# Kernel tuning notes

Measured on AMD Instinct MI355X. Metric: run time of the kernel, lower is better.

Reference implementation:

```python
import jax, jax.numpy as jnp
import numpy as np

D_MODEL = 1024
N_HEADS = 16
HEAD_DIM = D_MODEL // N_HEADS


def setup_inputs() -> dict:
    key = jax.random.key(0)
    ks = jax.random.split(key, 5)
    x = jax.random.normal(ks[0], (4, 2048, D_MODEL), dtype=jnp.float32)
    # qkv Linear: weight [3*d_model, d_model], bias [3*d_model]
    w_qkv = jax.random.normal(ks[1], (3 * D_MODEL, D_MODEL), dtype=jnp.float32) / np.sqrt(D_MODEL)
    b_qkv = jnp.zeros((3 * D_MODEL,), dtype=jnp.float32)
    w_out = jax.random.normal(ks[2], (D_MODEL, D_MODEL), dtype=jnp.float32) / np.sqrt(D_MODEL)
    b_out = jnp.zeros((D_MODEL,), dtype=jnp.float32)
    return {"x": x, "w_qkv": w_qkv, "b_qkv": b_qkv, "w_out": w_out, "b_out": b_out}


def reference(x, w_qkv, b_qkv, w_out, b_out):
    B, T, C = x.shape
    H, Dh = N_HEADS, HEAD_DIM
    qkv = x @ w_qkv.T + b_qkv                      # [B,T,3C]
    qkv = qkv.reshape(B, T, 3, H, Dh)
    q = jnp.transpose(qkv[:, :, 0], (0, 2, 1, 3))  # [B,H,T,Dh]
    k = jnp.transpose(qkv[:, :, 1], (0, 2, 1, 3))
    v = jnpp_transpose = jnp.transpose(qkv[:, :, 2], (0, 2, 1, 3))
    scale = 1.0 / np.sqrt(Dh).astype(np.float32)
    att = jnp.einsum('bhqd,bhkd->bhqk', q, k) * scale
    causal = jnp.tril(jnp.ones((T, T), dtype=bool))
    att = jnp.where(causal[None, None], att, -jnp.inf)
    att = jax.nn.softmax(att, axis=-1)
    head_out = jnp.einsum('bhqk,bhkd->bhqd', att, v)  # [B,H,T,Dh]
    out = jnp.transpose(head_out, (0, 2, 1, 3)).reshape(B, T, C)
    return out @ w_out.T + b_out
```

## Files before the change

kernel.cpp:

```cpp
#include <hip/hip_runtime.h>
#include <hip/hip_bf16.h>


#define D_MODEL 1024
#define N_HEADS 16
#define HEAD_DIM 64
#define SEQ 2048
#define BATCH 4

typedef __attribute__((ext_vector_type(8))) short bf16x8;
typedef __attribute__((ext_vector_type(4))) float f32x4;
typedef unsigned int uint;

__device__ __forceinline__ short f2bf(float f) {
    union { float f; uint i; } c; c.f = f;
    uint x = c.i;
    x += 0x7fffu + ((x >> 16) & 1u);
    return (short)(x >> 16);
}
__device__ __forceinline__ uint pack2(float a, float b) {
    return (uint)(unsigned short)f2bf(a) | ((uint)(unsigned short)f2bf(b) << 16);
}

__device__ __forceinline__ void glds16(const void* g, void* l) {
    __builtin_amdgcn_global_load_lds(
        (const __attribute__((address_space(1))) uint*)g,
        (__attribute__((address_space(3))) uint*)l, 16, 0, 0);
}

__global__ __launch_bounds__(256) void cvt_bf16(const float* __restrict__ src,
                                                short* __restrict__ dst, int n) {
    int i = (blockIdx.x * 256 + threadIdx.x) * 4;
    if (i < n) {
        float4 f = *(const float4*)(src + i);
        uint2 o; o.x = pack2(f.x, f.y); o.y = pack2(f.z, f.w);
        *(uint2*)(dst + i) = o;
    }
}

template <int MODE>
__global__ __launch_bounds__(256, 2) void gemm_bt(
    const short* __restrict__ A, const short* __restrict__ B,
    const float* __restrict__ bias, float* __restrict__ Cp,
    int M, int N, int K,
    short* __restrict__ qp, short* __restrict__ kp, short* __restrict__ vp)
{
    __shared__ short As[128][32];
    __shared__ short Bs[128][32];
    const int tid = threadIdx.x;
    const int wave = tid >> 6, lane = tid & 63;
    const int quad = lane >> 4, l16 = lane & 15;
    const int wm = (wave >> 1) * 64, wn = (wave & 1) * 64;
    const int rowBase = blockIdx.y * 128;
    const int colBase = blockIdx.x * 128;

    const short* gA = A + (size_t)(rowBase + wave * 32 + (lane >> 2)) * K + (lane & 3) * 8;
    const short* gB = B + (size_t)(colBase + wave * 32 + (lane >> 2)) * K + (lane & 3) * 8;
    void* lA0 = &As[wave * 32][0];
    void* lA1 = &As[wave * 32 + 16][0];
    void* lB0 = &Bs[wave * 32][0];
    void* lB1 = &Bs[wave * 32 + 16][0];

    f32x4 acc[4][4] = {};

    for (int k0 = 0; k0 < K; k0 += 32) {
        __syncthreads();
        glds16(gA + k0, lA0);
        glds16(gA + (size_t)16 * K + k0, lA1);
        glds16(gB + k0, lB0);
        glds16(gB + (size_t)16 * K + k0, lB1);
        __syncthreads();
        bf16x8 af[4], bfr[4];
#pragma unroll
        for (int i = 0; i < 4; ++i)
            af[i] = *(const bf16x8*)&As[wm + i * 16 + l16][quad * 8];
#pragma unroll
        for (int j = 0; j < 4; ++j)
            bfr[j] = *(const bf16x8*)&Bs[wn + j * 16 + l16][quad * 8];
#pragma unroll
        for (int i = 0; i < 4; ++i)
#pragma unroll
            for (int j = 0; j < 4; ++j)
                acc[i][j] = __builtin_amdgcn_mfma_f32_16x16x32_bf16(af[i], bfr[j], acc[i][j], 0, 0, 0);
    }

#pragma unroll
    for (int i = 0; i < 4; ++i) {
#pragma unroll
        for (int j = 0; j < 4; ++j) {
#pragma unroll
            for (int r = 0; r < 4; ++r) {
                int row = rowBase + wm + i * 16 + quad * 4 + r;
                int col = colBase + wn + j * 16 + l16;
                float v = acc[i][j][r] + bias[col];
                if (MODE == 0) {
                    Cp[(size_t)row * N + col] = v;
                } else {
                    int which = col >> 10;
                    int h = (col >> 6) & 15;
                    int d = col & 63;
                    int b = row >> 11;
                    int t = row & 2047;
                    short* dst = (which == 0) ? qp : (which == 1) ? kp : vp;
                    dst[((((size_t)b * N_HEADS + h) * SEQ) + t) * HEAD_DIM + d] = f2bf(v);
                }
            }
        }
    }
}

__global__ __launch_bounds__(256, 2) void attn_fwd(
    const short* __restrict__ Q, const short* __restrict__ K,
    const short* __restrict__ V, short* __restrict__ O)
{
    __shared__ short Ks[64][72];
    __shared__ short Vt[64][72];
    __shared__ short Ps[128][72];
    const int tid = threadIdx.x;
    const int wave = tid >> 6, lane = tid & 63;
    const int quad = lane >> 4, l16 = lane & 15;
    const int bh = blockIdx.y;
    const int b = bh >> 4, h = bh & 15;
    const int qbase = blockIdx.x * 128;
    const size_t hoff = (size_t)bh * SEQ * HEAD_DIM;
    const short* Qh = Q + hoff;
    const short* Kh = K + hoff;
    const short* Vh = V + hoff;

    bf16x8 qf[2][2];
#pragma unroll
    for (int m = 0; m < 2; ++m)
#pragma unroll
        for (int st = 0; st < 2; ++st)
            qf[m][st] = *(const bf16x8*)(Qh + (size_t)(qbase + wave * 32 + m * 16 + l16) * HEAD_DIM + st * 32 + quad * 8);

    f32x4 o[2][4] = {};
    float lsum[2][4] = {};
    const float scale = 0.125f;
    const float SHIFT = 10.0f;

    const int kr = tid >> 2, kc = (tid & 3) * 16;
    const int vk = (tid & 31) * 2, vd = (tid >> 5) * 8;

    const int ntiles = 2 * blockIdx.x + 2;
    for (int j = 0; j < ntiles; ++j) {
        const int kb = j * 64;
        int4 kv0 = *(const int4*)(Kh + (size_t)(kb + kr) * HEAD_DIM + kc);
        int4 kv1 = *(const int4*)(Kh + (size_t)(kb + kr) * HEAD_DIM + kc + 8);
        int4 vv0 = *(const int4*)(Vh + (size_t)(kb + vk) * HEAD_DIM + vd);
        int4 vv1 = *(const int4*)(Vh + (size_t)(kb + vk + 1) * HEAD_DIM + vd);
        __syncthreads();
        *(int4*)&Ks[kr][kc] = kv0;
        *(int4*)&Ks[kr][kc + 8] = kv1;
        {
            const short* va = (const short*)&vv0;
            const short* vb = (const short*)&vv1;
#pragma unroll
            for (int e = 0; e < 8; ++e)
                *(uint*)&Vt[vd + e][vk] =
                    (uint)(unsigned short)va[e] | ((uint)(unsigned short)vb[e] << 16);
        }
        __syncthreads();

        f32x4 s[2][4];
#pragma unroll
        for (int kt = 0; kt < 4; ++kt) {
            bf16x8 kf0 = *(const bf16x8*)&Ks[kt * 16 + l16][quad * 8];
            bf16x8 kf1 = *(const bf16x8*)&Ks[kt * 16 + l16][32 + quad * 8];
#pragma unroll
            for (int m = 0; m < 2; ++m) {
                f32x4 t = {0.f, 0.f, 0.f, 0.f};
                t = __builtin_amdgcn_mfma_f32_16x16x32_bf16(qf[m][0], kf0, t, 0, 0, 0);
                t = __builtin_amdgcn_mfma_f32_16x16x32_bf16(qf[m][1], kf1, t, 0, 0, 0);
                s[m][kt] = t;
            }
        }
#pragma unroll
        for (int m = 0; m < 2; ++m) {
            const int sub = qbase + wave * 32 + m * 16;
            const bool needmask = (kb + 63 > sub);
#pragma unroll
            for (int r = 0; r < 4; ++r) {
                int qrow = sub + quad * 4 + r;
                int prow = wave * 32 + m * 16 + quad * 4 + r;
#pragma unroll
                for (int kt = 0; kt < 4; ++kt) {
                    float a = s[m][kt][r] * scale - SHIFT;
                    if (needmask && (kb + kt * 16 + l16 > qrow)) a = -1e30f;
                    float p = __expf(a);
                    lsum[m][r] += p;
                    Ps[prow][kt * 16 + l16] = f2bf(p);
                }
            }
        }
#pragma unroll
        for (int st = 0; st < 2; ++st) {
            bf16x8 pf0 = *(const bf16x8*)&Ps[wave * 32 + l16][st * 32 + quad * 8];
            bf16x8 pf1 = *(const bf16x8*)&Ps[wave * 32 + 16 + l16][st * 32 + quad * 8];
#pragma unroll
            for (int dt = 0; dt < 4; ++dt) {
                bf16x8 vf = *(const bf16x8*)&Vt[dt * 16 + l16][st * 32 + quad * 8];
                o[0][dt] = __builtin_amdgcn_mfma_f32_16x16x32_bf16(pf0, vf, o[0][dt], 0, 0, 0);
                o[1][dt] = __builtin_amdgcn_mfma_f32_16x16x32_bf16(pf1, vf, o[1][dt], 0, 0, 0);
            }
        }
    }

#pragma unroll
    for (int m = 0; m < 2; ++m) {
#pragma unroll
        for (int r = 0; r < 4; ++r) {
            float l = lsum[m][r];
            l += __shfl_xor(l, 1);
            l += __shfl_xor(l, 2);
            l += __shfl_xor(l, 4);
            l += __shfl_xor(l, 8);
            float inv = 1.f / l;
            int t = qbase + wave * 32 + m * 16 + quad * 4 + r;
            size_t base = ((size_t)b * SEQ + t) * D_MODEL + h * HEAD_DIM;
#pragma unroll
            for (int dt = 0; dt < 4; ++dt)
                O[base + dt * 16 + l16] = f2bf(o[m][dt][r] * inv);
        }
    }
}

extern "C" void kernel_launch(void* const* d_in, const int* in_sizes, int n_in,
                              void* d_out, int out_size, void* d_ws, size_t ws_size,
                              hipStream_t stream)
{
    const float* x     = (const float*)d_in[0];
    const float* w_qkv = (const float*)d_in[1];
    const float* b_qkv = (const float*)d_in[2];
    const float* w_out = (const float*)d_in[3];
    const float* b_out = (const float*)d_in[4];
    float* out = (float*)d_out;

    const int NX = BATCH * SEQ * D_MODEL;
    const int NWQ = 3 * D_MODEL * D_MODEL;
    const int NWO = D_MODEL * D_MODEL;
    const size_t HE = (size_t)BATCH * N_HEADS * SEQ * HEAD_DIM;

    short* xb    = (short*)d_ws;
    short* wqkvb = xb + NX;
    short* woutb = wqkvb + NWQ;
    short* qp    = woutb + NWO;
    short* kp    = qp + HE;
    short* vp    = kp + HE;
    short* ho    = xb;

    const int M = BATCH * SEQ;

    cvt_bf16<<<NX / 1024, 256, 0, stream>>>(x, xb, NX);
    cvt_bf16<<<NWQ / 1024, 256, 0, stream>>>(w_qkv, wqkvb, NWQ);
    cvt_bf16<<<NWO / 1024, 256, 0, stream>>>(w_out, woutb, NWO);

    gemm_bt<1><<<dim3(3 * D_MODEL / 128, M / 128), 256, 0, stream>>>(
        xb, wqkvb, b_qkv, nullptr, M, 3 * D_MODEL, D_MODEL, qp, kp, vp);

    attn_fwd<<<dim3(SEQ / 128, BATCH * N_HEADS), 256, 0, stream>>>(qp, kp, vp, ho);

    gemm_bt<0><<<dim3(D_MODEL / 128, M / 128), 256, 0, stream>>>(
        ho, woutb, b_out, out, M, D_MODEL, D_MODEL, nullptr, nullptr, nullptr);
}
```

Measured before the change: 303.9 us.

## Store V transposed from QKV GEMM, read K from global, double-buffer V tile

The QKV GEMM epilogue now writes V in a [B,H,Dh,T] transposed layout, so attention can copy V tiles straight into shared memory without a per-element transpose. K fragments are loaded directly from global memory instead of being staged in LDS. V is double-buffered, which drops one barrier per tile, and the S MFMA operands are swapped so each lane owns a query column. That allows packed bf16 truncation stores of P, exp2 with a fused scale, and a simpler row-sum reduction. Heavy query tiles are scheduled first and occupancy is raised to 3 blocks per CU. The trade-offs are extra global K traffic, bf16 truncation instead of rounding for P, and scattered stores of transposed V in the epilogue.

```diff
diff --git a/kernel.cpp b/kernel.cpp
--- a/kernel.cpp
+++ b/kernel.cpp
@@ -20,6 +20,10 @@
 }
 __device__ __forceinline__ uint pack2(float a, float b) {
     return (uint)(unsigned short)f2bf(a) | ((uint)(unsigned short)f2bf(b) << 16);
+}
+__device__ __forceinline__ uint asu(float f) { union { float f; uint i; } c; c.f = f; return c.i; }
+__device__ __forceinline__ uint packtr(float lo, float hi) {
+    return (asu(lo) >> 16) | (asu(hi) & 0xffff0000u);
 }
 
 __device__ __forceinline__ void glds16(const void* g, void* l) {
@@ -101,31 +105,34 @@
                     int d = col & 63;
                     int b = row >> 11;
                     int t = row & 2047;
-                    short* dst = (which == 0) ? qp : (which == 1) ? kp : vp;
-                    dst[((((size_t)b * N_HEADS + h) * SEQ) + t) * HEAD_DIM + d] = f2bf(v);
+                    if (which == 2) {
+                        vp[((((size_t)b * N_HEADS + h) * HEAD_DIM) + d) * SEQ + t] = f2bf(v);
+                    } else {
+                        short* dst = (which == 0) ? qp : kp;
+                        dst[((((size_t)b * N_HEADS + h) * SEQ) + t) * HEAD_DIM + d] = f2bf(v);
+                    }
                 }
             }
         }
     }
 }
 
-__global__ __launch_bounds__(256, 2) void attn_fwd(
+__global__ __launch_bounds__(256, 3) void attn_fwd(
     const short* __restrict__ Q, const short* __restrict__ K,
-    const short* __restrict__ V, short* __restrict__ O)
+    const short* __restrict__ Vt_g, short* __restrict__ O)
 {
-    __shared__ short Ks[64][72];
-    __shared__ short Vt[64][72];
+    __shared__ short Vt[2][64][72];
     __shared__ short Ps[128][72];
     const int tid = threadIdx.x;
     const int wave = tid >> 6, lane = tid & 63;
     const int quad = lane >> 4, l16 = lane & 15;
     const int bh = blockIdx.y;
     const int b = bh >> 4, h = bh & 15;
-    const int qbase = blockIdx.x * 128;
-    const size_t hoff = (size_t)bh * SEQ * HEAD_DIM;
-    const short* Qh = Q + hoff;
-    const short* Kh = K + hoff;
-    const short* Vh = V + hoff;
+    const int qt = gridDim.x - 1 - blockIdx.x;
+    const int qbase = qt * 128;
+    const short* Qh = Q + (size_t)bh * SEQ * HEAD_DIM;
+    const short* Kh = K + (size_t)bh * SEQ * HEAD_DIM;
+    const short* Vh = Vt_g + (size_t)bh * HEAD_DIM * SEQ;
 
     bf16x8 qf[2][2];
 #pragma unroll
@@ -135,62 +142,54 @@
             qf[m][st] = *(const bf16x8*)(Qh + (size_t)(qbase + wave * 32 + m * 16 + l16) * HEAD_DIM + st * 32 + quad * 8);
 
     f32x4 o[2][4] = {};
-    float lsum[2][4] = {};
-    const float scale = 0.125f;
-    const float SHIFT = 10.0f;
-
-    const int kr = tid >> 2, kc = (tid & 3) * 16;
-    const int vk = (tid & 31) * 2, vd = (tid >> 5) * 8;
-
-    const int ntiles = 2 * blockIdx.x + 2;
+    float lsum[2] = {0.f, 0.f};
+    const float C1 = 0.125f * 1.44269504f;
+    const float C2 = 14.4269504f;
+
+    const int vr = tid >> 2, vc = (tid & 3) * 16;
+
+    const int ntiles = 2 * qt + 2;
     for (int j = 0; j < ntiles; ++j) {
         const int kb = j * 64;
-        int4 kv0 = *(const int4*)(Kh + (size_t)(kb + kr) * HEAD_DIM + kc);
-        int4 kv1 = *(const int4*)(Kh + (size_t)(kb + kr) * HEAD_DIM + kc + 8);
-        int4 vv0 = *(const int4*)(Vh + (size_t)(kb + vk) * HEAD_DIM + vd);
-        int4 vv1 = *(const int4*)(Vh + (size_t)(kb + vk + 1) * HEAD_DIM + vd);
+        int4 v0 = *(const int4*)(Vh + (size_t)vr * SEQ + kb + vc);
+        int4 v1 = *(const int4*)(Vh + (size_t)vr * SEQ + kb + vc + 8);
+        short(*vbuf)[72] = Vt[j & 1];
+        *(int4*)&vbuf[vr][vc] = v0;
+        *(int4*)&vbuf[vr][vc + 8] = v1;
         __syncthreads();
-        *(int4*)&Ks[kr][kc] = kv0;
-        *(int4*)&Ks[kr][kc + 8] = kv1;
-        {
-            const short* va = (const short*)&vv0;
-            const short* vb = (const short*)&vv1;
-#pragma unroll
-            for (int e = 0; e < 8; ++e)
-                *(uint*)&Vt[vd + e][vk] =
-                    (uint)(unsigned short)va[e] | ((uint)(unsigned short)vb[e] << 16);
-        }
-        __syncthreads();
-
+
+        const short* kbase = Kh + (size_t)(kb + l16) * HEAD_DIM + quad * 8;
         f32x4 s[2][4];
 #pragma unroll
         for (int kt = 0; kt < 4; ++kt) {
-            bf16x8 kf0 = *(const bf16x8*)&Ks[kt * 16 + l16][quad * 8];
-            bf16x8 kf1 = *(const bf16x8*)&Ks[kt * 16 + l16][32 + quad * 8];
+            bf16x8 kf0 = *(const bf16x8*)(kbase + kt * 16 * HEAD_DIM);
+            bf16x8 kf1 = *(const bf16x8*)(kbase + kt * 16 * HEAD_DIM + 32);
 #pragma unroll
             for (int m = 0; m < 2; ++m) {
                 f32x4 t = {0.f, 0.f, 0.f, 0.f};
-                t = __builtin_amdgcn_mfma_f32_16x16x32_bf16(qf[m][0], kf0, t, 0, 0, 0);
-                t = __builtin_amdgcn_mfma_f32_16x16x32_bf16(qf[m][1], kf1, t, 0, 0, 0);
+                t = __builtin_amdgcn_mfma_f32_16x16x32_bf16(kf0, qf[m][0], t, 0, 0, 0);
+                t = __builtin_amdgcn_mfma_f32_16x16x32_bf16(kf1, qf[m][1], t, 0, 0, 0);
                 s[m][kt] = t;
             }
         }
 #pragma unroll
         for (int m = 0; m < 2; ++m) {
             const int sub = qbase + wave * 32 + m * 16;
+            const int qrow = sub + l16;
             const bool needmask = (kb + 63 > sub);
-#pragma unroll
-            for (int r = 0; r < 4; ++r) {
-                int qrow = sub + quad * 4 + r;
-                int prow = wave * 32 + m * 16 + quad * 4 + r;
-#pragma unroll
-                for (int kt = 0; kt < 4; ++kt) {
-                    float a = s[m][kt][r] * scale - SHIFT;
-                    if (needmask && (kb + kt * 16 + l16 > qrow)) a = -1e30f;
-                    float p = __expf(a);
-                    lsum[m][r] += p;
-                    Ps[prow][kt * 16 + l16] = f2bf(p);
+            const int prow = wave * 32 + m * 16 + l16;
+#pragma unroll
+            for (int kt = 0; kt < 4; ++kt) {
+                float p[4];
+#pragma unroll
+                for (int r = 0; r < 4; ++r) {
+                    float a = __builtin_fmaf(s[m][kt][r], C1, -C2);
+                    if (needmask && (kb + kt * 16 + quad * 4 + r > qrow)) a = -1e30f;
+                    p[r] = __builtin_exp2f(a);
+                    lsum[m] += p[r];
                 }
+                uint2 u; u.x = packtr(p[0], p[1]); u.y = packtr(p[2], p[3]);
+                *(uint2*)&Ps[prow][kt * 16 + quad * 4] = u;
             }
         }
 #pragma unroll
@@ -199,7 +198,7 @@
             bf16x8 pf1 = *(const bf16x8*)&Ps[wave * 32 + 16 + l16][st * 32 + quad * 8];
 #pragma unroll
             for (int dt = 0; dt < 4; ++dt) {
-                bf16x8 vf = *(const bf16x8*)&Vt[dt * 16 + l16][st * 32 + quad * 8];
+                bf16x8 vf = *(const bf16x8*)&vbuf[dt * 16 + l16][st * 32 + quad * 8];
                 o[0][dt] = __builtin_amdgcn_mfma_f32_16x16x32_bf16(pf0, vf, o[0][dt], 0, 0, 0);
                 o[1][dt] = __builtin_amdgcn_mfma_f32_16x16x32_bf16(pf1, vf, o[1][dt], 0, 0, 0);
             }
@@ -208,15 +207,15 @@
 
 #pragma unroll
     for (int m = 0; m < 2; ++m) {
+        float l = lsum[m];
+        l += __shfl_xor(l, 16);
+        l += __shfl_xor(l, 32);
 #pragma unroll
         for (int r = 0; r < 4; ++r) {
-            float l = lsum[m][r];
-            l += __shfl_xor(l, 1);
-            l += __shfl_xor(l, 2);
-            l += __shfl_xor(l, 4);
-            l += __shfl_xor(l, 8);
-            float inv = 1.f / l;
-            int t = qbase + wave * 32 + m * 16 + quad * 4 + r;
+            int qloc = quad * 4 + r;
+            float lq = __shfl(l, qloc);
+            float inv = 1.f / lq;
+            int t = qbase + wave * 32 + m * 16 + qloc;
             size_t base = ((size_t)b * SEQ + t) * D_MODEL + h * HEAD_DIM;
 #pragma unroll
             for (int dt = 0; dt < 4; ++dt)
```

New measurement: 364.6 us. 1.2x slower.
